# Performance work log

Measured on AMD Instinct MI355X. Metric: run time of the kernel, lower is better.

The kernel has to match this reference:

```python
import jax, jax.numpy as jnp
import numpy as np

D_MODEL = 768
NUM_HEADS = 12
D_K = D_MODEL // NUM_HEADS
WINDOW = 16
SPARSITY = 0.8
NEG = -1e9


def _pos_encoding(seq_len, d_model, dtype):
    pos = jnp.arange(seq_len, dtype=jnp.float32)[:, None]
    div = jnp.exp(jnp.arange(0, d_model, 2, dtype=jnp.float32) * (-np.log(10000.0) / d_model))
    pe = jnp.zeros((seq_len, d_model), dtype=jnp.float32)
    pe = pe.at[:, 0::2].set(jnp.sin(pos * div))
    pe = pe.at[:, 1::2].set(jnp.cos(pos * div))
    return pe.astype(dtype)


def _layernorm(x, gamma, beta, eps=1e-5):
    mu = jnp.mean(x, axis=-1, keepdims=True)
    var = jnp.mean(jnp.square(x - mu), axis=-1, keepdims=True)
    return (x - mu) * jax.lax.rsqrt(var + eps) * gamma + beta


def _split_heads(x):  # [B,S,D] -> [B,H,S,dk]
    b, s, _ = x.shape
    return x.reshape(b, s, NUM_HEADS, D_K).transpose(0, 2, 1, 3)


def _attn(q, k, v, mask):  # mask broadcastable to [B,H,S,S], bool
    scores = jnp.einsum('bhqd,bhkd->bhqk', q, k) / jnp.sqrt(jnp.asarray(D_K, q.dtype))
    scores = jnp.where(mask, scores, jnp.asarray(NEG, q.dtype))
    w = jax.nn.softmax(scores, axis=-1)
    out = jnp.einsum('bhqk,bhkd->bhqd', w, v)
    b, h, s, d = out.shape
    return out.transpose(0, 2, 1, 3).reshape(b, s, h * d)


def setup_inputs() -> dict:
    key = jax.random.key(0)
    ks = jax.random.split(key, 16)
    d = D_MODEL
    sc = 1.0 / np.sqrt(d)
    inp = {
        'x': jax.random.normal(ks[0], (2, 2048, d), jnp.float32),
        'wgq': jax.random.normal(ks[1], (d, d), jnp.float32) * sc,
        'wgk': jax.random.normal(ks[2], (d, d), jnp.float32) * sc,
        'wgv': jax.random.normal(ks[3], (d, d), jnp.float32) * sc,
        'wlq': jax.random.normal(ks[4], (d, d), jnp.float32) * sc,
        'wlk': jax.random.normal(ks[5], (d, d), jnp.float32) * sc,
        'wlv': jax.random.normal(ks[6], (d, d), jnp.float32) * sc,
        'wtq': jax.random.normal(ks[7], (d, d), jnp.float32) * sc,
        'wtk': jax.random.normal(ks[8], (d, d), jnp.float32) * sc,
        'wtv': jax.random.normal(ks[9], (d, d), jnp.float32) * sc,
        'w_out': jax.random.normal(ks[10], (3 * d, d), jnp.float32) * (1.0 / np.sqrt(3 * d)),
        'b_out': jnp.zeros((d,), jnp.float32),
        'w_gate': jax.random.normal(ks[11], (d, 3), jnp.float32) * sc,
        'b_gate': jnp.zeros((3,), jnp.float32),
        'w_sparse': jax.random.normal(ks[12], (d, 1), jnp.float32) * sc,
        'b_sparse': jnp.zeros((1,), jnp.float32),
        'g_gamma': jnp.ones((d,), jnp.float32), 'g_beta': jnp.zeros((d,), jnp.float32),
        'l_gamma': jnp.ones((d,), jnp.float32), 'l_beta': jnp.zeros((d,), jnp.float32),
        't_gamma': jnp.ones((d,), jnp.float32), 't_beta': jnp.zeros((d,), jnp.float32),
    }
    return inp


def reference(x, wgq, wgk, wgv, wlq, wlk, wlv, wtq, wtk, wtv,
              w_out, b_out, w_gate, b_gate, w_sparse, b_sparse,
              g_gamma, g_beta, l_gamma, l_beta, t_gamma, t_beta):
    b, s, d = x.shape
    # positional encoding branch input (dropout is identity at eval)
    x_pos = x + _pos_encoding(s, d, x.dtype)[None]

    # focus gate over mean-pooled tokens -> [B,3]
    fw = jax.nn.softmax(x.mean(axis=1) @ w_gate + b_gate, axis=-1)
    gw, lw, tw = fw[:, 0, None, None], fw[:, 1, None, None], fw[:, 2, None, None]

    # sparse (global) mask: keep top-k important columns per batch
    importance = (x @ w_sparse + b_sparse)[..., 0]  # [B,S]
    k = max(1, int((1.0 - SPARSITY) * s))
    _, topk_idx = jax.lax.top_k(importance, k)
    sparse = jnp.zeros((b, s), bool).at[jnp.arange(b)[:, None], topk_idx].set(True)
    sparse_mask = sparse[:, None, None, :]  # [B,1,1,S]

    idx = jnp.arange(s)
    rel = idx[None, :] - idx[:, None]
    half = WINDOW // 2
    local_mask = ((rel >= -half) & (rel <= half))[None, None]  # [1,1,S,S]

    stride = max(1, s // 8)
    temporal_cols = (idx % stride) == 0
    temporal_mask = jnp.broadcast_to(temporal_cols[None, :], (s, s))[None, None]

    # global branch
    g = _attn(_split_heads(x @ wgq), _split_heads(x @ wgk), _split_heads(x @ wgv), sparse_mask)
    g = _layernorm(g, g_gamma, g_beta)
    # local branch
    l = _attn(_split_heads(x @ wlq), _split_heads(x @ wlk), _split_heads(x @ wlv), local_mask)
    l = _layernorm(l, l_gamma, l_beta)
    # temporal branch (uses pos-encoded input)
    t = _attn(_split_heads(x_pos @ wtq), _split_heads(x_pos @ wtk), _split_heads(x_pos @ wtv), temporal_mask)
    t = _layernorm(t, t_gamma, t_beta)

    combined = jnp.concatenate([g * gw, l * lw, t * tw], axis=-1)
    return combined @ w_out + b_out
```

## Files before the change

### kernel.cpp

```cpp
#include <hip/hip_runtime.h>
#include <cstdint>

constexpr int BB   = 2;
constexpr int SS   = 2048;
constexpr int DD   = 768;
constexpr int HH   = 12;
constexpr int NTOK = BB * SS;
constexpr int KSEL = 409;
constexpr int KPAD = 448;
constexpr int NKT  = 7;

typedef __bf16 bf16x8 __attribute__((ext_vector_type(8)));
typedef float  f32x4  __attribute__((ext_vector_type(4)));

__device__ __forceinline__ float b2f(unsigned short u) {
  return __uint_as_float(((unsigned)u) << 16);
}
__device__ __forceinline__ unsigned short f2b(float f) {
  unsigned u = __float_as_uint(f);
  u += 0x7fffu + ((u >> 16) & 1u);
  return (unsigned short)(u >> 16);
}
__device__ __forceinline__ unsigned long long shfl_xor_u64(unsigned long long v, int m) {
  unsigned lo = (unsigned)v, hi = (unsigned)(v >> 32);
  lo = __shfl_xor(lo, m, 64);
  hi = __shfl_xor(hi, m, 64);
  return ((unsigned long long)hi << 32) | lo;
}

__device__ __forceinline__ void gload_lds16(const void* gsrc, void* ldst) {
  __builtin_amdgcn_global_load_lds(
      (__attribute__((address_space(1))) void*)(gsrc),
      (__attribute__((address_space(3))) void*)(ldst), 16, 0, 0);
}

__global__ __launch_bounds__(256) void mega_pre(
    const float* __restrict__ x, const float* __restrict__ wsp,
    const float* __restrict__ bsp,
    unsigned short* __restrict__ xb, unsigned short* __restrict__ xpb,
    float* __restrict__ imp,
    const float* w0, const float* w1, const float* w2, const float* w3,
    const float* w4, const float* w5, const float* w6, const float* w7,
    const float* w8, const float* w9,
    unsigned short* __restrict__ WTx4, unsigned short* __restrict__ WTkv,
    unsigned short* __restrict__ WTqt, unsigned short* __restrict__ WTtkv,
    unsigned short* __restrict__ WTo,
    float* __restrict__ partial) {
  __shared__ float tile[32][33];
  int id = blockIdx.x;
  int tid = threadIdx.x;

  if (id < SS) {
    int srow = id;
    const float* xr0 = x + (long)srow * DD;
    const float* xr1 = x + (long)(SS + srow) * DD;
    float acc0 = 0.f, acc1 = 0.f;
#pragma unroll
    for (int k = 0; k < 3; ++k) {
      int c = tid + k * 256;
      int j2 = c & ~1;
      float freq = __expf((float)j2 * -0.011992630692677323f);
      float ang = (float)srow * freq;
      float pe = (c & 1) ? cosf(ang) : sinf(ang);
      float w = wsp[c];
      float x0 = xr0[c], x1 = xr1[c];
      xb[(long)srow * DD + c]        = f2b(x0);
      xb[(long)(SS + srow) * DD + c] = f2b(x1);
      xpb[(long)srow * DD + c]        = f2b(x0 + pe);
      xpb[(long)(SS + srow) * DD + c] = f2b(x1 + pe);
      acc0 += x0 * w;
      acc1 += x1 * w;
    }
#pragma unroll
    for (int m = 1; m < 64; m <<= 1) {
      acc0 += __shfl_xor(acc0, m, 64);
      acc1 += __shfl_xor(acc1, m, 64);
    }
    __shared__ float red[8];
    int wv = tid >> 6, lane = tid & 63;
    if (lane == 0) { red[wv] = acc0; red[4 + wv] = acc1; }
    __syncthreads();
    if (tid == 0) {
      imp[srow]      = red[0] + red[1] + red[2] + red[3] + bsp[0];
      imp[SS + srow] = red[4] + red[5] + red[6] + red[7] + bsp[0];
    }
  } else if (id < SS + 6912) {
    int tidx = id - SS;
    int z, bx, by;
    if (tidx < 5184) { z = tidx / 576; int rem = tidx % 576; by = rem / 24; bx = rem % 24; }
    else             { z = 9; int rem = tidx - 5184; by = rem / 24; bx = rem % 24; }
    const float* srcs[10] = {w0, w1, w2, w3, w4, w5, w6, w7, w8, w9};
    const float* src = srcs[z];
    unsigned short* dst;
    int R = DD;
    switch (z) {
      case 0: dst = WTx4;                       break;
      case 1: dst = WTkv;                       break;
      case 2: dst = WTkv + (long)DD * DD;       break;
      case 3: dst = WTx4 + (long)DD * DD;       break;
      case 4: dst = WTx4 + (long)2 * DD * DD;   break;
      case 5: dst = WTx4 + (long)3 * DD * DD;   break;
      case 6: dst = WTqt;                       break;
      case 7: dst = WTtkv;                      break;
      case 8: dst = WTtkv + (long)DD * DD;      break;
      default: dst = WTo; R = 2304;             break;
    }
    int r0 = by * 32, c0 = bx * 32;
    int tx = tid & 31, ty = tid >> 5;
    for (int i = ty; i < 32; i += 8) tile[i][tx] = src[(long)(r0 + i) * DD + c0 + tx];
    __syncthreads();
    for (int i = ty; i < 32; i += 8) dst[(long)(c0 + i) * R + r0 + tx] = f2b(tile[tx][i]);
  } else {
    int rem = id - SS - 6912;
    int chunk = rem & 15, b = rem >> 4;
    for (int c = tid; c < DD; c += 256) {
      const float* xp = x + ((long)(b * SS + chunk * 128)) * DD + c;
      float acc = 0.f;
      for (int s2 = 0; s2 < 128; ++s2) acc += xp[(long)s2 * DD];
      partial[(long)(b * 16 + chunk) * DD + c] = acc;
    }
  }
}

__global__ __launch_bounds__(1024) void topk_gate2(
    const float* __restrict__ imp, int* __restrict__ sel,
    const float* __restrict__ partial, const float* __restrict__ w_gate,
    const float* __restrict__ b_gate, float* __restrict__ fw) {
  int tid = threadIdx.x;
  if (blockIdx.x < 2) {
    __shared__ unsigned long long keys[SS];
    int b = blockIdx.x;
    for (int i = tid; i < SS; i += 1024) {
      float v = imp[b * SS + i];
      unsigned u = __float_as_uint(v);
      u = (u & 0x80000000u) ? ~u : (u | 0x80000000u);
      unsigned du = ~u;
      keys[i] = ((unsigned long long)du << 32) | (unsigned)i;
    }
    __syncthreads();
    for (int k = 2; k <= SS; k <<= 1) {
      for (int j = k >> 1; j >= 64; j >>= 1) {
        for (int i = tid; i < SS; i += 1024) {
          int p = i ^ j;
          if (p > i) {
            unsigned long long a = keys[i], bb = keys[p];
            bool up = ((i & k) == 0);
            if ((a > bb) == up) { keys[i] = bb; keys[p] = a; }
          }
        }
        __syncthreads();
      }
      unsigned long long k0 = keys[tid], k1 = keys[tid + 1024];
      bool up0 = ((tid & k) == 0);
      bool up1 = (((tid + 1024) & k) == 0);
      int j0 = (k >> 1) < 32 ? (k >> 1) : 32;
      for (int j = j0; j >= 1; j >>= 1) {
        bool low = ((tid & j) == 0);
        unsigned long long p0 = shfl_xor_u64(k0, j);
        k0 = ((low == up0) == (k0 < p0)) ? k0 : p0;
        unsigned long long p1 = shfl_xor_u64(k1, j);
        k1 = ((low == up1) == (k1 < p1)) ? k1 : p1;
      }
      keys[tid] = k0; keys[tid + 1024] = k1;
      __syncthreads();
    }
    for (int i = tid; i < KSEL; i += 1024) sel[b * KSEL + i] = (int)(keys[i] & 0xffffffffu);
  } else {
    __shared__ float meanbuf[DD];
    __shared__ float lg[3];
    int b = blockIdx.x - 2;
    if (tid < DD) {
      float acc = 0.f;
      for (int p = 0; p < 16; ++p) acc += partial[(long)(b * 16 + p) * DD + tid];
      meanbuf[tid] = acc * (1.0f / (float)SS);
    }
    __syncthreads();
    if (tid < 3) {
      float acc = b_gate[tid];
      for (int d = 0; d < DD; ++d) acc += meanbuf[d] * w_gate[d * 3 + tid];
      lg[tid] = acc;
    }
    __syncthreads();
    if (tid == 0) {
      float mx = fmaxf(lg[0], fmaxf(lg[1], lg[2]));
      float e0 = expf(lg[0] - mx), e1 = expf(lg[1] - mx), e2 = expf(lg[2] - mx);
      float inv = 1.f / (e0 + e1 + e2);
      fw[b * 3 + 0] = e0 * inv; fw[b * 3 + 1] = e1 * inv; fw[b * 3 + 2] = e2 * inv;
    }
  }
}

__global__ __launch_bounds__(256) void gemm_multi(
    const unsigned short* __restrict__ xb,    const unsigned short* __restrict__ WTx4,
    unsigned short* __restrict__ QKV4,
    const unsigned short* __restrict__ WTkv,  unsigned short* __restrict__ KVg,
    const unsigned short* __restrict__ xpb,   const unsigned short* __restrict__ WTqt,
    unsigned short* __restrict__ Qt,
    const unsigned short* __restrict__ WTtkv,
    const int* __restrict__ sel,
    unsigned short* __restrict__ K8, unsigned short* __restrict__ Vt8,
    unsigned short* __restrict__ Vt, unsigned short* __restrict__ Vtl) {
  __shared__ unsigned short AsB[2][4096];
  __shared__ unsigned short BsB[2][4096];
  constexpr int K = DD;
  const int tid = threadIdx.x;
  const int lane = tid & 63;
  const int wv = tid >> 6;
  const int wr = wv >> 1, wc = wv & 1;

  int lin = blockIdx.x;
  int xcd = lin & 7, idx = lin >> 3;
  const unsigned short* BT;
  int ntx, tile, region;
  if (idx < 96) {
    region = 0; BT = WTx4; ntx = 24;
    int r = (xcd >> 2) * 16 + (idx & 15);
    int c = (xcd & 3) * 6 + (idx >> 4);
    tile = r * 24 + c;
  } else {
    int e = xcd * 36 + (idx - 96);
    if (e < 84)       { region = 1; BT = WTkv;  ntx = 12; tile = e; }
    else if (e < 276) { region = 2; BT = WTqt;  ntx = 6;  tile = e - 84; }
    else              { region = 3; BT = WTtkv; ntx = 12; tile = e - 276; }
  }
  const long rowBase = (long)(tile / ntx) * 128;
  const long colBase = (long)(tile % ntx) * 128;

  auto arow = [&](int r) -> const unsigned short* {
    long grow = rowBase + r;
    if (region == 0) return xb + grow * (long)K;
    if (region == 2) return xpb + grow * (long)K;
    if (region == 1) {
      int bb2 = (int)(grow / KPAD), j = (int)(grow % KPAD);
      int srow = (j < KSEL) ? sel[bb2 * KSEL + j] : 0;
      return xb + ((long)bb2 * SS + srow) * (long)K;
    }
    if (grow < 16) {
      int bb2 = (int)grow >> 3, j = ((int)grow & 7) * 256;
      return xpb + ((long)bb2 * SS + j) * (long)K;
    }
    return xpb;
  };

  f32x4 acc[4][4];
#pragma unroll
  for (int i = 0; i < 4; ++i)
#pragma unroll
    for (int j = 0; j < 4; ++j)
#pragma unroll
      for (int r = 0; r < 4; ++r) acc[i][j][r] = 0.f;

  const int g0 = tid, g1 = tid + 256;
  const int r0 = g0 >> 2, k80 = (g0 & 3) ^ ((r0 >> 1) & 3);
  const int r1 = g1 >> 2, k81 = (g1 & 3) ^ ((r1 >> 1) & 3);
  const unsigned short* ga0 = arow(r0) + k80 * 8;
  const unsigned short* ga1 = arow(r1) + k81 * 8;
  const unsigned short* gb0 = BT + (colBase + r0) * (long)K + k80 * 8;
  const unsigned short* gb1 = BT + (colBase + r1) * (long)K + k81 * 8;

  const int k8 = lane >> 4;
  const int fr = lane & 15;
  int aoff[4], boff[4];
#pragma unroll
  for (int i = 0; i < 4; ++i) {
    int rowA = wr * 64 + i * 16 + fr;
    aoff[i] = (rowA * 4 + (k8 ^ ((rowA >> 1) & 3))) * 8;
    int rowB = wc * 64 + i * 16 + fr;
    boff[i] = (rowB * 4 + (k8 ^ ((rowB >> 1) & 3))) * 8;
  }

  auto stage = [&](int buf, int t) {
    int ko = t * 32;
    gload_lds16(ga0 + ko, &AsB[buf][g0 * 8]);
    gload_lds16(ga1 + ko, &AsB[buf][g1 * 8]);
    gload_lds16(gb0 + ko, &BsB[buf][g0 * 8]);
    gload_lds16(gb1 + ko, &BsB[buf][g1 * 8]);
  };

  constexpr int nk = K >> 5;
  stage(0, 0);
  __syncthreads();
  for (int t = 0; t < nk; ++t) {
    int cur = t & 1;
    if (t + 1 < nk) stage(cur ^ 1, t + 1);
    bf16x8 af[4], bfr[4];
#pragma unroll
    for (int i = 0; i < 4; ++i) af[i] = *(const bf16x8*)(&AsB[cur][aoff[i]]);
#pragma unroll
    for (int i = 0; i < 4; ++i) bfr[i] = *(const bf16x8*)(&BsB[cur][boff[i]]);
#pragma unroll
    for (int mi = 0; mi < 4; ++mi)
#pragma unroll
      for (int ni = 0; ni < 4; ++ni)
        acc[mi][ni] = __builtin_amdgcn_mfma_f32_16x16x32_bf16(af[mi], bfr[ni], acc[mi][ni], 0, 0, 0);
    __syncthreads();
  }

  int mode, vcol0 = 0, N = 0;
  unsigned short* C = nullptr;
  if (region == 0)      { mode = (colBase >= 2304) ? 1 : 0; C = QKV4; N = 3072;
                          vcol0 = (int)colBase - 2304; }
  else if (region == 1) { mode = (colBase >= 768) ? 2 : 0;  C = KVg;  N = 1536;
                          vcol0 = (int)colBase - 768; }
  else if (region == 2) { mode = 0; C = Qt; N = 768; }
  else                  { mode = (colBase >= 768) ? 4 : 3;
                          vcol0 = (int)colBase - 768; }

  const int orow0 = (lane >> 4) * 4;
  if (mode == 0) {
#pragma unroll
    for (int mi = 0; mi < 4; ++mi) {
      long gr = rowBase + wr * 64 + mi * 16 + orow0;
#pragma unroll
      for (int ni = 0; ni < 4; ++ni) {
        long gc = colBase + wc * 64 + ni * 16 + fr;
#pragma unroll
        for (int r = 0; r < 4; ++r)
          C[(gr + r) * (long)N + gc] = f2b(acc[mi][ni][r]);
      }
    }
  } else {
#pragma unroll
    for (int mi = 0; mi < 4; ++mi) {
      int lr = wr * 64 + mi * 16 + orow0;
      int grow = (int)rowBase + lr;
#pragma unroll
      for (int ni = 0; ni < 4; ++ni) {
        int lc = wc * 64 + ni * 16 + fr;
        uint2 pk;
        pk.x = (unsigned)f2b(acc[mi][ni][0]) | ((unsigned)f2b(acc[mi][ni][1]) << 16);
        pk.y = (unsigned)f2b(acc[mi][ni][2]) | ((unsigned)f2b(acc[mi][ni][3]) << 16);
        if (mode == 1) {
          int bb2 = grow >> 11, s = grow & (SS - 1);
          *(uint2*)(Vtl + ((long)bb2 * DD + vcol0 + lc) * SS + s) = pk;
        } else if (mode == 2) {
          int bb2 = grow / KPAD, j = grow - bb2 * KPAD;
          *(uint2*)(Vt + ((long)bb2 * DD + vcol0 + lc) * KPAD + j) = pk;
        } else if (mode == 3) {
          if (grow < 16) {
#pragma unroll
            for (int r = 0; r < 4; ++r) {
              int g2 = grow + r;
              K8[((long)(g2 >> 3) * 16 + (g2 & 7)) * DD + colBase + lc] =
                  f2b(acc[mi][ni][r]);
            }
          }
        } else {
          if (grow < 16) {
            *(uint2*)(Vt8 + ((long)(grow >> 3) * DD + vcol0 + lc) * 32 + (grow & 7)) = pk;
          }
        }
      }
    }
    if (mode == 4) {
#pragma unroll
      for (int e = 0; e < 6; ++e) {
        int id = tid + e * 256;
        int bb2 = id / 768, rem = id % 768;
        int c = rem / 6, ch = rem % 6;
        *(uint2*)(Vt8 + ((long)bb2 * DD + vcol0 + c) * 32 + 8 + ch * 4) = uint2{0u, 0u};
      }
    }
  }
}

__global__ __launch_bounds__(256) void gemm_final_sk(const unsigned short* __restrict__ A,
                                                     const unsigned short* __restrict__ BT,
                                                     float* __restrict__ Cpart) {
  __shared__ unsigned short As[2][128 * 32];
  __shared__ unsigned short Bs[2][128 * 32];
  constexpr int N = 768, K = 2304, CK = 768;
  const int tid = threadIdx.x;
  const int lane = tid & 63;
  const int wv = tid >> 6;
  const int wr = wv >> 1, wc = wv & 1;
  const int z = blockIdx.z;

  int lin = blockIdx.y * gridDim.x + blockIdx.x;
  int swz = (lin & 7) * 24 + (lin >> 3);
  const long rowBase = (long)(swz / 6) * 128;
  const long colBase = (long)(swz % 6) * 128;

  f32x4 acc[4][4];
#pragma unroll
  for (int i = 0; i < 4; ++i)
#pragma unroll
    for (int j = 0; j < 4; ++j)
#pragma unroll
      for (int r = 0; r < 4; ++r) acc[i][j][r] = 0.f;

  const int g0 = tid, g1 = tid + 256;
  const int r0 = g0 >> 2, k80 = (g0 & 3) ^ ((r0 >> 1) & 3);
  const int r1 = g1 >> 2, k81 = (g1 & 3) ^ ((r1 >> 1) & 3);
  const unsigned short* ga0 = A + (rowBase + r0) * (long)K + z * CK + k80 * 8;
  const unsigned short* ga1 = A + (rowBase + r1) * (long)K + z * CK + k81 * 8;
  const unsigned short* gb0 = BT + (colBase + r0) * (long)K + z * CK + k80 * 8;
  const unsigned short* gb1 = BT + (colBase + r1) * (long)K + z * CK + k81 * 8;

  const int k8 = lane >> 4;
  const int fr = lane & 15;
  int aoff[4], boff[4];
#pragma unroll
  for (int i = 0; i < 4; ++i) {
    int rowA = wr * 64 + i * 16 + fr;
    aoff[i] = (rowA * 4 + (k8 ^ ((rowA >> 1) & 3))) * 8;
    int rowB = wc * 64 + i * 16 + fr;
    boff[i] = (rowB * 4 + (k8 ^ ((rowB >> 1) & 3))) * 8;
  }

  auto stage = [&](int buf, int t) {
    int ko = t * 32;
    gload_lds16(ga0 + ko, &As[buf][g0 * 8]);
    gload_lds16(ga1 + ko, &As[buf][g1 * 8]);
    gload_lds16(gb0 + ko, &Bs[buf][g0 * 8]);
    gload_lds16(gb1 + ko, &Bs[buf][g1 * 8]);
  };

  constexpr int nk = CK >> 5;
  stage(0, 0);
  __syncthreads();
  for (int t = 0; t < nk; ++t) {
    int cur = t & 1;
    if (t + 1 < nk) stage(cur ^ 1, t + 1);
    bf16x8 af[4], bfr[4];
#pragma unroll
    for (int i = 0; i < 4; ++i) af[i] = *(const bf16x8*)(&As[cur][aoff[i]]);
#pragma unroll
    for (int i = 0; i < 4; ++i) bfr[i] = *(const bf16x8*)(&Bs[cur][boff[i]]);
#pragma unroll
    for (int mi = 0; mi < 4; ++mi)
#pragma unroll
      for (int ni = 0; ni < 4; ++ni)
        acc[mi][ni] = __builtin_amdgcn_mfma_f32_16x16x32_bf16(af[mi], bfr[ni], acc[mi][ni], 0, 0, 0);
    __syncthreads();
  }

  float* Cz = Cpart + (long)z * NTOK * DD;
  const int orow0 = (lane >> 4) * 4;
#pragma unroll
  for (int mi = 0; mi < 4; ++mi) {
    long gr = rowBase + wr * 64 + mi * 16 + orow0;
#pragma unroll
    for (int ni = 0; ni < 4; ++ni) {
      long gc = colBase + wc * 64 + ni * 16 + fr;
#pragma unroll
      for (int r = 0; r < 4; ++r)
        Cz[(gr + r) * (long)N + gc] = acc[mi][ni][r];
    }
  }
}

__global__ __launch_bounds__(256) void reduce_out(const float* __restrict__ P,
                                                  const float* __restrict__ bias,
                                                  float* __restrict__ out) {
  long i = (long)blockIdx.x * 256 + threadIdx.x;
  const f32x4* p0 = (const f32x4*)P;
  const f32x4* p1 = (const f32x4*)(P + (long)NTOK * DD);
  const f32x4* p2 = (const f32x4*)(P + 2L * NTOK * DD);
  f32x4 v = p0[i];
  v += p1[i];
  v += p2[i];
  int c4 = (int)(i % (DD / 4));
  v += *(const f32x4*)(bias + c4 * 4);
  ((f32x4*)out)[i] = v;
}

__device__ __forceinline__ void attn_flash_body(
    const unsigned short* __restrict__ QKV4,
    const unsigned short* __restrict__ KVg,
    const unsigned short* __restrict__ Vt,
    unsigned short* __restrict__ comb,
    unsigned short* smem) {
  unsigned short* Kl = smem;
  unsigned short* Vl = smem + 8192;
  unsigned short* Pl = smem + 16384;
  int tid = threadIdx.x, w = tid >> 6, lane = tid & 63;
  int fr = lane & 15, g = lane >> 4;
  int b = blockIdx.y / HH, h = blockIdx.y % HH, hoff = h * 64;
  int qbase = blockIdx.x * 64 + w * 16;
  long qrow = (long)b * SS + qbase + fr;

  const unsigned short* qptr = QKV4 + qrow * 3072 + hoff + g * 8;
  bf16x8 bq0 = *(const bf16x8*)(qptr);
  bf16x8 bq1 = *(const bf16x8*)(qptr + 32);

  const int s0 = tid, s1 = tid + 256;
  const int r0 = s0 >> 3, c0 = (s0 & 7) ^ (r0 & 7);
  const int r1 = s1 >> 3, c1 = (s1 & 7) ^ (r1 & 7);
  const unsigned short* kg_b = KVg + (long)b * KPAD * 1536 + hoff;
  const unsigned short* vt_b = Vt + ((long)b * DD + hoff) * KPAD;

  auto stage = [&](int buf, int t0) {
    gload_lds16(kg_b + (long)(t0 * 64 + r0) * 1536 + c0 * 8, &Kl[buf * 4096 + s0 * 8]);
    gload_lds16(kg_b + (long)(t0 * 64 + r1) * 1536 + c1 * 8, &Kl[buf * 4096 + s1 * 8]);
    gload_lds16(vt_b + (long)r0 * KPAD + t0 * 64 + c0 * 8, &Vl[buf * 4096 + s0 * 8]);
    gload_lds16(vt_b + (long)r1 * KPAD + t0 * 64 + c1 * 8, &Vl[buf * 4096 + s1 * 8]);
  };

  f32x4 oacc[4];
#pragma unroll
  for (int mf = 0; mf < 4; ++mf)
#pragma unroll
    for (int r = 0; r < 4; ++r) oacc[mf][r] = 0.f;
  float m = -3.0e38f, l = 0.f;

  stage(0, 0);
  asm volatile("s_waitcnt vmcnt(0)" ::: "memory");
  __syncthreads();

  for (int t = 0; t < NKT; ++t) {
    int cur = t & 1;
    if (t + 1 < NKT) stage(cur ^ 1, t + 1);

    f32x4 st[4];
#pragma unroll
    for (int kt = 0; kt < 4; ++kt) {
      int row = kt * 16 + fr;
      bf16x8 a0 = *(const bf16x8*)(&Kl[cur * 4096 + (row * 8 + (g ^ (row & 7))) * 8]);
      bf16x8 a1 = *(const bf16x8*)(&Kl[cur * 4096 + (row * 8 + ((4 + g) ^ (row & 7))) * 8]);
      f32x4 z = {0.f, 0.f, 0.f, 0.f};
      z = __builtin_amdgcn_mfma_f32_16x16x32_bf16(a0, bq0, z, 0, 0, 0);
      st[kt] = __builtin_amdgcn_mfma_f32_16x16x32_bf16(a1, bq1, z, 0, 0, 0);
    }

    float tm = -3.0e38f;
#pragma unroll
    for (int kt = 0; kt < 4; ++kt)
#pragma unroll
      for (int r = 0; r < 4; ++r) {
        int key = t * 64 + kt * 16 + g * 4 + r;
        float s = (key < KSEL) ? st[kt][r] * 0.125f : -1.0e30f;
        st[kt][r] = s;
        tm = fmaxf(tm, s);
      }
    tm = fmaxf(tm, __shfl_xor(tm, 16, 64));
    tm = fmaxf(tm, __shfl_xor(tm, 32, 64));
    float newm = fmaxf(m, tm);
    float f = __expf(m - newm);
    float tsum = 0.f;
#pragma unroll
    for (int kt = 0; kt < 4; ++kt)
#pragma unroll
      for (int r = 0; r < 4; ++r) {
        float e = __expf(st[kt][r] - newm);
        st[kt][r] = e;
        tsum += e;
      }
    tsum += __shfl_xor(tsum, 16, 64);
    tsum += __shfl_xor(tsum, 32, 64);
    l = l * f + tsum;
    m = newm;
#pragma unroll
    for (int mf = 0; mf < 4; ++mf)
#pragma unroll
      for (int r = 0; r < 4; ++r) oacc[mf][r] *= f;

    unsigned short* pw = &Pl[w * 1088 + fr * 68 + g * 4];
#pragma unroll
    for (int kt = 0; kt < 4; ++kt) {
      uint2 pk;
      pk.x = (unsigned)f2b(st[kt][0]) | ((unsigned)f2b(st[kt][1]) << 16);
      pk.y = (unsigned)f2b(st[kt][2]) | ((unsigned)f2b(st[kt][3]) << 16);
      *(uint2*)(pw + kt * 16) = pk;
    }

    const unsigned short* prd = &Pl[w * 1088 + fr * 68];
#pragma unroll
    for (int ks2 = 0; ks2 < 2; ++ks2) {
      bf16x8 pf = *(const bf16x8*)(prd + ks2 * 32 + g * 8);
#pragma unroll
      for (int mf = 0; mf < 4; ++mf) {
        int vr = mf * 16 + fr;
        int vc = ks2 * 4 + g;
        bf16x8 vf = *(const bf16x8*)(&Vl[cur * 4096 + (vr * 8 + (vc ^ (vr & 7))) * 8]);
        oacc[mf] = __builtin_amdgcn_mfma_f32_16x16x32_bf16(vf, pf, oacc[mf], 0, 0, 0);
      }
    }

    asm volatile("s_waitcnt vmcnt(0)" ::: "memory");
    __syncthreads();
  }

  float inv = 1.f / l;
  unsigned short* orow = comb + qrow * 2304 + hoff;
#pragma unroll
  for (int mf = 0; mf < 4; ++mf) {
    uint2 pk;
    pk.x = (unsigned)f2b(oacc[mf][0] * inv) | ((unsigned)f2b(oacc[mf][1] * inv) << 16);
    pk.y = (unsigned)f2b(oacc[mf][2] * inv) | ((unsigned)f2b(oacc[mf][3] * inv) << 16);
    *(uint2*)(orow + mf * 16 + g * 4) = pk;
  }
}

__device__ __forceinline__ void attn_win_body(
    const unsigned short* __restrict__ QKV,
    const unsigned short* __restrict__ K8,
    const unsigned short* __restrict__ Vt,
    unsigned short* __restrict__ comb, int brOff,
    int LD, int QO, long VSTR, bool local,
    unsigned short* smem) {
  int tid = threadIdx.x, w = tid >> 6, lane = tid & 63;
  int fr = lane & 15, g = lane >> 4;
  int b = blockIdx.y / HH, h = blockIdx.y % HH, hoff = h * 64;
  int qbase = blockIdx.x * 64 + w * 16;
  long qrow = (long)b * SS + qbase + fr;

  const unsigned short* qptr = QKV + qrow * LD + QO + hoff + g * 8;
  bf16x8 bq0 = *(const bf16x8*)(qptr);
  bf16x8 bq1 = *(const bf16x8*)(qptr + 32);

  int kstart = qbase - 8;
  if (kstart < 0) kstart = 0;
  if (kstart > SS - 32) kstart = SS - 32;

  f32x4 st[2];
  if (local) {
#pragma unroll
    for (int kt = 0; kt < 2; ++kt) {
      const unsigned short* kp =
          QKV + ((long)b * SS + kstart + kt * 16 + fr) * LD + 1536 + hoff + g * 8;
      bf16x8 a0 = *(const bf16x8*)(kp);
      bf16x8 a1 = *(const bf16x8*)(kp + 32);
      f32x4 z = {0.f, 0.f, 0.f, 0.f};
      z = __builtin_amdgcn_mfma_f32_16x16x32_bf16(a0, bq0, z, 0, 0, 0);
      st[kt] = __builtin_amdgcn_mfma_f32_16x16x32_bf16(a1, bq1, z, 0, 0, 0);
    }
  } else {
    const unsigned short* kp = K8 + ((long)b * 16 + fr) * DD + hoff + g * 8;
    bf16x8 a0 = *(const bf16x8*)(kp);
    bf16x8 a1 = *(const bf16x8*)(kp + 32);
    f32x4 z = {0.f, 0.f, 0.f, 0.f};
    z = __builtin_amdgcn_mfma_f32_16x16x32_bf16(a0, bq0, z, 0, 0, 0);
    st[0] = __builtin_amdgcn_mfma_f32_16x16x32_bf16(a1, bq1, z, 0, 0, 0);
    st[1] = f32x4{0.f, 0.f, 0.f, 0.f};
  }

  float m = -3.0e38f;
#pragma unroll
  for (int kt = 0; kt < 2; ++kt)
#pragma unroll
    for (int r = 0; r < 4; ++r) {
      int idx = kt * 16 + g * 4 + r;
      bool valid;
      if (local) {
        int rel = kstart + idx - qbase - fr;
        valid = (rel >= -8) && (rel <= 8);
      } else {
        valid = (idx < 8);
      }
      float s = valid ? st[kt][r] * 0.125f : -1.0e30f;
      st[kt][r] = s;
      m = fmaxf(m, s);
    }
  m = fmaxf(m, __shfl_xor(m, 16, 64));
  m = fmaxf(m, __shfl_xor(m, 32, 64));

  float lsum = 0.f;
#pragma unroll
  for (int kt = 0; kt < 2; ++kt)
#pragma unroll
    for (int r = 0; r < 4; ++r) {
      float e = __expf(st[kt][r] - m);
      st[kt][r] = e;
      lsum += e;
    }
  lsum += __shfl_xor(lsum, 16, 64);
  lsum += __shfl_xor(lsum, 32, 64);

  unsigned short* pl = smem + w * 640 + fr * 40 + g * 4;
#pragma unroll
  for (int kt = 0; kt < 2; ++kt) {
    uint2 pk;
    pk.x = (unsigned)f2b(st[kt][0]) | ((unsigned)f2b(st[kt][1]) << 16);
    pk.y = (unsigned)f2b(st[kt][2]) | ((unsigned)f2b(st[kt][3]) << 16);
    *(uint2*)(pl + kt * 16) = pk;
  }

  f32x4 oacc[4];
#pragma unroll
  for (int mf = 0; mf < 4; ++mf)
#pragma unroll
    for (int r = 0; r < 4; ++r) oacc[mf][r] = 0.f;

  const unsigned short* pr = smem + w * 640 + fr * 40 + g * 8;
  bf16x8 pf = *(const bf16x8*)(pr);
  long kb2 = local ? kstart : 0;
#pragma unroll
  for (int mf = 0; mf < 4; ++mf) {
    const unsigned short* vp =
        Vt + ((long)b * DD + hoff + mf * 16 + fr) * VSTR + kb2 + g * 8;
    bf16x8 vf = *(const bf16x8*)(vp);
    oacc[mf] = __builtin_amdgcn_mfma_f32_16x16x32_bf16(vf, pf, oacc[mf], 0, 0, 0);
  }

  float inv = 1.f / lsum;
  unsigned short* orow = comb + qrow * 2304 + brOff + hoff;
#pragma unroll
  for (int mf = 0; mf < 4; ++mf) {
    uint2 pk;
    pk.x = (unsigned)f2b(oacc[mf][0] * inv) | ((unsigned)f2b(oacc[mf][1] * inv) << 16);
    pk.y = (unsigned)f2b(oacc[mf][2] * inv) | ((unsigned)f2b(oacc[mf][3] * inv) << 16);
    *(uint2*)(orow + mf * 16 + g * 4) = pk;
  }
}

__global__ __launch_bounds__(256) void attn_all(
    const unsigned short* __restrict__ QKV4,
    const unsigned short* __restrict__ KVg,
    const unsigned short* __restrict__ Vt,
    const unsigned short* __restrict__ Qt,
    const unsigned short* __restrict__ K8,
    const unsigned short* __restrict__ Vt8,
    const unsigned short* __restrict__ Vtl,
    unsigned short* __restrict__ comb) {
  __shared__ unsigned short smem[20736];
  int z = blockIdx.z;
  if (z == 0) {
    attn_flash_body(QKV4, KVg, Vt, comb, smem);
  } else if (z == 1) {
    attn_win_body(QKV4, nullptr, Vtl, comb, 768, 3072, 768, SS, true, smem);
  } else {
    attn_win_body(Qt, K8, Vt8, comb, 1536, 768, 0, 32, false, smem);
  }
}

__global__ __launch_bounds__(256) void ln_gate_inplace(
    unsigned short* __restrict__ comb,
    const float* __restrict__ gg, const float* __restrict__ gb,
    const float* __restrict__ lgam, const float* __restrict__ lbet,
    const float* __restrict__ tg, const float* __restrict__ tb,
    const float* __restrict__ fw) {
  int row = blockIdx.x;
  int b = row >> 11;
  int tid = threadIdx.x;
  __shared__ float red[8];
  const float* gams[3] = {gg, lgam, tg};
  const float* bets[3] = {gb, lbet, tb};
#pragma unroll
  for (int br = 0; br < 3; ++br) {
    unsigned short* p = comb + (long)row * 2304 + br * DD;
    float x0 = b2f(p[tid]), x1 = b2f(p[tid + 256]), x2 = b2f(p[tid + 512]);
    float s = x0 + x1 + x2;
    float ss = x0 * x0 + x1 * x1 + x2 * x2;
#pragma unroll
    for (int msk = 1; msk < 64; msk <<= 1) {
      s += __shfl_xor(s, msk, 64);
      ss += __shfl_xor(ss, msk, 64);
    }
    int wv = tid >> 6, lane = tid & 63;
    if (lane == 0) { red[wv] = s; red[4 + wv] = ss; }
    __syncthreads();
    float S4 = red[0] + red[1] + red[2] + red[3];
    float SQ = red[4] + red[5] + red[6] + red[7];
    float mean = S4 * (1.f / (float)DD);
    float var = SQ * (1.f / (float)DD) - mean * mean;
    float rs = rsqrtf(var + 1e-5f);
    float gate = fw[b * 3 + br];
    const float* gam = gams[br];
    const float* bet = bets[br];
    p[tid]       = f2b(((x0 - mean) * rs * gam[tid]       + bet[tid])       * gate);
    p[tid + 256] = f2b(((x1 - mean) * rs * gam[tid + 256] + bet[tid + 256]) * gate);
    p[tid + 512] = f2b(((x2 - mean) * rs * gam[tid + 512] + bet[tid + 512]) * gate);
    __syncthreads();
  }
}

extern "C" void kernel_launch(void* const* d_in, const int* in_sizes, int n_in,
                              void* d_out, int out_size, void* d_ws, size_t ws_size,
                              hipStream_t stream) {
  const float* x        = (const float*)d_in[0];
  const float* wgq      = (const float*)d_in[1];
  const float* wgk      = (const float*)d_in[2];
  const float* wgv      = (const float*)d_in[3];
  const float* wlq      = (const float*)d_in[4];
  const float* wlk      = (const float*)d_in[5];
  const float* wlv      = (const float*)d_in[6];
  const float* wtq      = (const float*)d_in[7];
  const float* wtk      = (const float*)d_in[8];
  const float* wtv      = (const float*)d_in[9];
  const float* w_out    = (const float*)d_in[10];
  const float* b_out    = (const float*)d_in[11];
  const float* w_gate   = (const float*)d_in[12];
  const float* b_gate   = (const float*)d_in[13];
  const float* w_sparse = (const float*)d_in[14];
  const float* b_sparse = (const float*)d_in[15];
  const float* g_gamma  = (const float*)d_in[16];
  const float* g_beta   = (const float*)d_in[17];
  const float* l_gamma  = (const float*)d_in[18];
  const float* l_beta   = (const float*)d_in[19];
  const float* t_gamma  = (const float*)d_in[20];
  const float* t_beta   = (const float*)d_in[21];
  float* outp = (float*)d_out;

  unsigned short* xb    = (unsigned short*)d_ws;
  unsigned short* xpb   = xb    + (long)NTOK * DD;
  unsigned short* WTx4  = xpb   + (long)NTOK * DD;
  unsigned short* WTkv  = WTx4  + (long)3072 * DD;
  unsigned short* WTqt  = WTkv  + (long)1536 * DD;
  unsigned short* WTtkv = WTqt  + (long)DD * DD;
  unsigned short* WTo   = WTtkv + (long)1536 * DD;
  unsigned short* QKV4  = WTo   + (long)DD * 2304;
  unsigned short* Qt    = QKV4  + (long)NTOK * 3072;
  unsigned short* KVg   = Qt    + (long)NTOK * DD;
  unsigned short* K8    = KVg   + (long)BB * KPAD * 1536;
  unsigned short* Vt8   = K8    + (long)BB * 16 * DD;
  unsigned short* Vt    = Vt8   + (long)BB * DD * 32;
  unsigned short* Vtl   = Vt    + (long)BB * DD * KPAD;
  unsigned short* comb  = Vtl   + (long)BB * DD * SS;
  float* Cpart   = (float*)(comb + (long)NTOK * 2304);
  float* imp     = Cpart + 3L * NTOK * DD;
  float* partial = imp + NTOK;
  float* fw      = partial + 32 * DD;
  int*   sel     = (int*)(fw + 8);

  mega_pre<<<SS + 6912 + 32, 256, 0, stream>>>(
      x, w_sparse, b_sparse, xb, xpb, imp,
      wgq, wgk, wgv, wlq, wlk, wlv, wtq, wtk, wtv, w_out,
      WTx4, WTkv, WTqt, WTtkv, WTo, partial);
  topk_gate2<<<4, 1024, 0, stream>>>(imp, sel, partial, w_gate, b_gate, fw);

  gemm_multi<<<1056, 256, 0, stream>>>(xb, WTx4, QKV4, WTkv, KVg,
                                       xpb, WTqt, Qt, WTtkv, sel,
                                       K8, Vt8, Vt, Vtl);

  attn_all<<<dim3(32, BB * HH, 3), 256, 0, stream>>>(QKV4, KVg, Vt, Qt, K8, Vt8,
                                                     Vtl, comb);

  ln_gate_inplace<<<NTOK, 256, 0, stream>>>(comb, g_gamma, g_beta,
                                            l_gamma, l_beta, t_gamma, t_beta, fw);
  gemm_final_sk<<<dim3(6, 32, 3), 256, 0, stream>>>(comb, WTo, Cpart);
  reduce_out<<<NTOK * DD / 4 / 256, 256, 0, stream>>>(Cpart, b_out, outp);
}
```

Baseline: 173.7 us.

## Fold LayerNorm and gate into output GEMM epilogue via row statistics

Removes the separate in-place LayerNorm+gate pass over the combined attention output. Gamma is folded into the transposed output weights, and the attention kernels accumulate per-row sum and sum-of-squares with atomics. The final reduction then applies mean, rstd, gate, and precomputed gamma·W and beta·W vectors algebraically. This saves one full read/write of the bf16 combined buffer and a launch. In exchange it adds a memset, atomics in the attention epilogue, and a serial 768-long dot-product loop in three extra topk blocks. It also uses E[x²]-mean² variance computed from pre-rounded fp32 values.

```diff
diff --git a/kernel.cpp b/kernel.cpp
--- a/kernel.cpp
+++ b/kernel.cpp
@@ -42,6 +42,8 @@
     const float* w0, const float* w1, const float* w2, const float* w3,
     const float* w4, const float* w5, const float* w6, const float* w7,
     const float* w8, const float* w9,
+    const float* __restrict__ gg, const float* __restrict__ lgam,
+    const float* __restrict__ tg,
     unsigned short* __restrict__ WTx4, unsigned short* __restrict__ WTkv,
     unsigned short* __restrict__ WTqt, unsigned short* __restrict__ WTtkv,
     unsigned short* __restrict__ WTo,
@@ -109,7 +111,13 @@
     int tx = tid & 31, ty = tid >> 5;
     for (int i = ty; i < 32; i += 8) tile[i][tx] = src[(long)(r0 + i) * DD + c0 + tx];
     __syncthreads();
-    for (int i = ty; i < 32; i += 8) dst[(long)(c0 + i) * R + r0 + tx] = f2b(tile[tx][i]);
+    float gamv = 1.f;
+    if (z == 9) {
+      int kk = r0 + tx;
+      gamv = (kk < 768) ? gg[kk] : (kk < 1536) ? lgam[kk - 768] : tg[kk - 1536];
+    }
+    for (int i = ty; i < 32; i += 8)
+      dst[(long)(c0 + i) * R + r0 + tx] = f2b(tile[tx][i] * gamv);
   } else {
     int rem = id - SS - 6912;
     int chunk = rem & 15, b = rem >> 4;
@@ -125,7 +133,13 @@
 __global__ __launch_bounds__(1024) void topk_gate2(
     const float* __restrict__ imp, int* __restrict__ sel,
     const float* __restrict__ partial, const float* __restrict__ w_gate,
-    const float* __restrict__ b_gate, float* __restrict__ fw) {
+    const float* __restrict__ b_gate, float* __restrict__ fw,
+    const float* __restrict__ w_out,
+    const float* __restrict__ gg, const float* __restrict__ lgam,
+    const float* __restrict__ tg,
+    const float* __restrict__ gb, const float* __restrict__ lbet,
+    const float* __restrict__ tb,
+    float* __restrict__ Sbuf, float* __restrict__ Tbuf) {
   int tid = threadIdx.x;
   if (blockIdx.x < 2) {
     __shared__ unsigned long long keys[SS];
@@ -165,7 +179,7 @@
       __syncthreads();
     }
     for (int i = tid; i < KSEL; i += 1024) sel[b * KSEL + i] = (int)(keys[i] & 0xffffffffu);
-  } else {
+  } else if (blockIdx.x < 4) {
     __shared__ float meanbuf[DD];
     __shared__ float lg[3];
     int b = blockIdx.x - 2;
@@ -186,6 +200,20 @@
       float e0 = expf(lg[0] - mx), e1 = expf(lg[1] - mx), e2 = expf(lg[2] - mx);
       float inv = 1.f / (e0 + e1 + e2);
       fw[b * 3 + 0] = e0 * inv; fw[b * 3 + 1] = e1 * inv; fw[b * 3 + 2] = e2 * inv;
+    }
+  } else {
+    int br = blockIdx.x - 4;
+    if (tid < DD) {
+      const float* gam = (br == 0) ? gg : (br == 1) ? lgam : tg;
+      const float* bet = (br == 0) ? gb : (br == 1) ? lbet : tb;
+      float accS = 0.f, accT = 0.f;
+      for (int k = 0; k < DD; ++k) {
+        float w = w_out[(long)(br * DD + k) * DD + tid];
+        accS += gam[k] * w;
+        accT += bet[k] * w;
+      }
+      Sbuf[br * DD + tid] = accS;
+      Tbuf[br * DD + tid] = accT;
     }
   }
 }
@@ -452,17 +480,33 @@
 
 __global__ __launch_bounds__(256) void reduce_out(const float* __restrict__ P,
                                                   const float* __restrict__ bias,
+                                                  const float* __restrict__ sumb,
+                                                  const float* __restrict__ sqb,
+                                                  const float* __restrict__ Sbuf,
+                                                  const float* __restrict__ Tbuf,
+                                                  const float* __restrict__ fw,
                                                   float* __restrict__ out) {
   long i = (long)blockIdx.x * 256 + threadIdx.x;
-  const f32x4* p0 = (const f32x4*)P;
-  const f32x4* p1 = (const f32x4*)(P + (long)NTOK * DD);
-  const f32x4* p2 = (const f32x4*)(P + 2L * NTOK * DD);
-  f32x4 v = p0[i];
-  v += p1[i];
-  v += p2[i];
+  int r = (int)(i / (DD / 4));
   int c4 = (int)(i % (DD / 4));
-  v += *(const f32x4*)(bias + c4 * 4);
-  ((f32x4*)out)[i] = v;
+  int b = r >> 11;
+  f32x4 o = *(const f32x4*)(bias + c4 * 4);
+#pragma unroll
+  for (int br = 0; br < 3; ++br) {
+    float sum = sumb[br * NTOK + r];
+    float sq  = sqb[br * NTOK + r];
+    float mean = sum * (1.f / (float)DD);
+    float var  = sq * (1.f / (float)DD) - mean * mean;
+    float rs   = rsqrtf(var + 1e-5f);
+    float gate = fw[b * 3 + br];
+    f32x4 P4 = ((const f32x4*)(P + (long)br * NTOK * DD))[i];
+    f32x4 S4 = *(const f32x4*)(Sbuf + br * DD + c4 * 4);
+    f32x4 T4 = *(const f32x4*)(Tbuf + br * DD + c4 * 4);
+#pragma unroll
+    for (int e = 0; e < 4; ++e)
+      o[e] += gate * (rs * (P4[e] - mean * S4[e]) + T4[e]);
+  }
+  ((f32x4*)out)[i] = o;
 }
 
 __device__ __forceinline__ void attn_flash_body(
@@ -470,6 +514,7 @@
     const unsigned short* __restrict__ KVg,
     const unsigned short* __restrict__ Vt,
     unsigned short* __restrict__ comb,
+    float* __restrict__ sumb, float* __restrict__ sqb,
     unsigned short* smem) {
   unsigned short* Kl = smem;
   unsigned short* Vl = smem + 8192;
@@ -583,12 +628,25 @@
 
   float inv = 1.f / l;
   unsigned short* orow = comb + qrow * 2304 + hoff;
+  float rsum = 0.f, rsq = 0.f;
 #pragma unroll
   for (int mf = 0; mf < 4; ++mf) {
+    float v0 = oacc[mf][0] * inv, v1 = oacc[mf][1] * inv;
+    float v2 = oacc[mf][2] * inv, v3 = oacc[mf][3] * inv;
+    rsum += v0 + v1 + v2 + v3;
+    rsq  += v0 * v0 + v1 * v1 + v2 * v2 + v3 * v3;
     uint2 pk;
-    pk.x = (unsigned)f2b(oacc[mf][0] * inv) | ((unsigned)f2b(oacc[mf][1] * inv) << 16);
-    pk.y = (unsigned)f2b(oacc[mf][2] * inv) | ((unsigned)f2b(oacc[mf][3] * inv) << 16);
+    pk.x = (unsigned)f2b(v0) | ((unsigned)f2b(v1) << 16);
+    pk.y = (unsigned)f2b(v2) | ((unsigned)f2b(v3) << 16);
     *(uint2*)(orow + mf * 16 + g * 4) = pk;
+  }
+  rsum += __shfl_xor(rsum, 16, 64);
+  rsum += __shfl_xor(rsum, 32, 64);
+  rsq  += __shfl_xor(rsq, 16, 64);
+  rsq  += __shfl_xor(rsq, 32, 64);
+  if (lane < 16) {
+    atomicAdd(&sumb[qrow], rsum);
+    atomicAdd(&sqb[qrow], rsq);
   }
 }
 
@@ -597,6 +655,7 @@
     const unsigned short* __restrict__ K8,
     const unsigned short* __restrict__ Vt,
     unsigned short* __restrict__ comb, int brOff,
+    float* __restrict__ sumb, float* __restrict__ sqb,
     int LD, int QO, long VSTR, bool local,
     unsigned short* smem) {
   int tid = threadIdx.x, w = tid >> 6, lane = tid & 63;
@@ -695,12 +754,25 @@
 
   float inv = 1.f / lsum;
   unsigned short* orow = comb + qrow * 2304 + brOff + hoff;
+  float rsum = 0.f, rsq = 0.f;
 #pragma unroll
   for (int mf = 0; mf < 4; ++mf) {
+    float v0 = oacc[mf][0] * inv, v1 = oacc[mf][1] * inv;
+    float v2 = oacc[mf][2] * inv, v3 = oacc[mf][3] * inv;
+    rsum += v0 + v1 + v2 + v3;
+    rsq  += v0 * v0 + v1 * v1 + v2 * v2 + v3 * v3;
     uint2 pk;
-    pk.x = (unsigned)f2b(oacc[mf][0] * inv) | ((unsigned)f2b(oacc[mf][1] * inv) << 16);
-    pk.y = (unsigned)f2b(oacc[mf][2] * inv) | ((unsigned)f2b(oacc[mf][3] * inv) << 16);
+    pk.x = (unsigned)f2b(v0) | ((unsigned)f2b(v1) << 16);
+    pk.y = (unsigned)f2b(v2) | ((unsigned)f2b(v3) << 16);
     *(uint2*)(orow + mf * 16 + g * 4) = pk;
+  }
+  rsum += __shfl_xor(rsum, 16, 64);
+  rsum += __shfl_xor(rsum, 32, 64);
+  rsq  += __shfl_xor(rsq, 16, 64);
+  rsq  += __shfl_xor(rsq, 32, 64);
+  if (lane < 16) {
+    atomicAdd(&sumb[qrow], rsum);
+    atomicAdd(&sqb[qrow], rsq);
   }
 }
 
@@ -712,56 +784,18 @@
     const unsigned short* __restrict__ K8,
     const unsigned short* __restrict__ Vt8,
     const unsigned short* __restrict__ Vtl,
-    unsigned short* __restrict__ comb) {
+    unsigned short* __restrict__ comb,
+    float* __restrict__ sumb, float* __restrict__ sqb) {
   __shared__ unsigned short smem[20736];
   int z = blockIdx.z;
   if (z == 0) {
-    attn_flash_body(QKV4, KVg, Vt, comb, smem);
+    attn_flash_body(QKV4, KVg, Vt, comb, sumb, sqb, smem);
   } else if (z == 1) {
-    attn_win_body(QKV4, nullptr, Vtl, comb, 768, 3072, 768, SS, true, smem);
+    attn_win_body(QKV4, nullptr, Vtl, comb, 768, sumb + NTOK, sqb + NTOK,
+                  3072, 768, SS, true, smem);
   } else {
-    attn_win_body(Qt, K8, Vt8, comb, 1536, 768, 0, 32, false, smem);
-  }
-}
-
-__global__ __launch_bounds__(256) void ln_gate_inplace(
-    unsigned short* __restrict__ comb,
-    const float* __restrict__ gg, const float* __restrict__ gb,
-    const float* __restrict__ lgam, const float* __restrict__ lbet,
-    const float* __restrict__ tg, const float* __restrict__ tb,
-    const float* __restrict__ fw) {
-  int row = blockIdx.x;
-  int b = row >> 11;
-  int tid = threadIdx.x;
-  __shared__ float red[8];
-  const float* gams[3] = {gg, lgam, tg};
-  const float* bets[3] = {gb, lbet, tb};
-#pragma unroll
-  for (int br = 0; br < 3; ++br) {
-    unsigned short* p = comb + (long)row * 2304 + br * DD;
-    float x0 = b2f(p[tid]), x1 = b2f(p[tid + 256]), x2 = b2f(p[tid + 512]);
-    float s = x0 + x1 + x2;
-    float ss = x0 * x0 + x1 * x1 + x2 * x2;
-#pragma unroll
-    for (int msk = 1; msk < 64; msk <<= 1) {
-      s += __shfl_xor(s, msk, 64);
-      ss += __shfl_xor(ss, msk, 64);
-    }
-    int wv = tid >> 6, lane = tid & 63;
-    if (lane == 0) { red[wv] = s; red[4 + wv] = ss; }
-    __syncthreads();
-    float S4 = red[0] + red[1] + red[2] + red[3];
-    float SQ = red[4] + red[5] + red[6] + red[7];
-    float mean = S4 * (1.f / (float)DD);
-    float var = SQ * (1.f / (float)DD) - mean * mean;
-    float rs = rsqrtf(var + 1e-5f);
-    float gate = fw[b * 3 + br];
-    const float* gam = gams[br];
-    const float* bet = bets[br];
-    p[tid]       = f2b(((x0 - mean) * rs * gam[tid]       + bet[tid])       * gate);
-    p[tid + 256] = f2b(((x1 - mean) * rs * gam[tid + 256] + bet[tid + 256]) * gate);
-    p[tid + 512] = f2b(((x2 - mean) * rs * gam[tid + 512] + bet[tid + 512]) * gate);
-    __syncthreads();
+    attn_win_body(Qt, K8, Vt8, comb, 1536, sumb + 2 * NTOK, sqb + 2 * NTOK,
+                  768, 0, 32, false, smem);
   }
 }
 
@@ -812,22 +846,30 @@
   float* partial = imp + NTOK;
   float* fw      = partial + 32 * DD;
   int*   sel     = (int*)(fw + 8);
+  float* sumb    = (float*)(sel + 1024);
+  float* sqb     = sumb + 3 * NTOK;
+  float* Sbuf    = sqb + 3 * NTOK;
+  float* Tbuf    = Sbuf + 3 * DD;
+
+  hipMemsetAsync(sumb, 0, (size_t)6 * NTOK * sizeof(float), stream);
 
   mega_pre<<<SS + 6912 + 32, 256, 0, stream>>>(
       x, w_sparse, b_sparse, xb, xpb, imp,
       wgq, wgk, wgv, wlq, wlk, wlv, wtq, wtk, wtv, w_out,
+      g_gamma, l_gamma, t_gamma,
       WTx4, WTkv, WTqt, WTtkv, WTo, partial);
-  topk_gate2<<<4, 1024, 0, stream>>>(imp, sel, partial, w_gate, b_gate, fw);
+  topk_gate2<<<7, 1024, 0, stream>>>(imp, sel, partial, w_gate, b_gate, fw,
+                                     w_out, g_gamma, l_gamma, t_gamma,
+                                     g_beta, l_beta, t_beta, Sbuf, Tbuf);
 
   gemm_multi<<<1056, 256, 0, stream>>>(xb, WTx4, QKV4, WTkv, KVg,
                                        xpb, WTqt, Qt, WTtkv, sel,
                                        K8, Vt8, Vt, Vtl);
 
   attn_all<<<dim3(32, BB * HH, 3), 256, 0, stream>>>(QKV4, KVg, Vt, Qt, K8, Vt8,
-                                                     Vtl, comb);
-
-  ln_gate_inplace<<<NTOK, 256, 0, stream>>>(comb, g_gamma, g_beta,
-                                            l_gamma, l_beta, t_gamma, t_beta, fw);
+                                                     Vtl, comb, sumb, sqb);
+
   gemm_final_sk<<<dim3(6, 32, 3), 256, 0, stream>>>(comb, WTo, Cpart);
-  reduce_out<<<NTOK * DD / 4 / 256, 256, 0, stream>>>(Cpart, b_out, outp);
-}
+  reduce_out<<<NTOK * DD / 4 / 256, 256, 0, stream>>>(Cpart, b_out, sumb, sqb,
+                                                      Sbuf, Tbuf, fw, outp);
+}
```

New measurement: 195.2 us. +12.4%, slower.
